# Optimization experiments

Hardware: AMD Instinct MI355X
Metric: run time of the kernel (lower is better)

Reference implementation:

```python
import jax, jax.numpy as jnp
import numpy as np

LEAKAGE = 0.9
RADIUS = 0.1
AVG_DEGREE = 6


def setup_inputs() -> dict:
    key = jax.random.key(0)
    k1, k2, k3, k4, k5 = jax.random.split(key, 5)
    B, T, I, N, O = 16, 2048, 32, 2048, 32
    input_sequence = jax.random.normal(k1, (B, T, I), dtype=jnp.float32)
    # sparse reservoir matrix, uniform(-1,1) with density avg_degree/N, scaled to spectral radius
    A = jax.random.uniform(k2, (N, N), minval=-1.0, maxval=1.0, dtype=jnp.float32)
    mask = jax.random.uniform(k3, (N, N)) < (AVG_DEGREE / N)
    A = jnp.where(mask, A, 0.0)
    # approximate spectral normalization (power-iteration-free surrogate scale)
    A = A * (RADIUS / jnp.max(jnp.abs(jnp.linalg.eigvals(A))).astype(jnp.float32))
    Win = (RADIUS) * (2.0 * jax.random.uniform(k4, (N, I), dtype=jnp.float32) - 1.0)
    Wout_w = jax.random.normal(k5, (O, N), dtype=jnp.float32) / np.sqrt(N)
    return {"input_sequence": input_sequence, "Win": Win, "A": A, "Wout_w": Wout_w, "washout_len": 64}


def reference(input_sequence, Win, A, Wout_w, washout_len):
    # input projection for all timesteps at once (noise_std = 0.0)
    inp = jnp.einsum('bti,ni->btn', input_sequence, Win)  # [B, T, N]
    B = input_sequence.shape[0]
    N = A.shape[0]
    h0 = jnp.zeros((B, N), dtype=input_sequence.dtype)
    At = A.T

    def step(h, u_t):
        # h: [B, N], u_t: [B, N]
        h_new = (1.0 - LEAKAGE) * h + LEAKAGE * jnp.tanh(h @ At + u_t)
        return h_new, h_new

    _, hs = jax.lax.scan(step, h0, jnp.swapaxes(inp, 0, 1))  # hs: [T, B, N]
    hs = jnp.swapaxes(hs, 0, 1)  # [B, T, N]
    h_list = hs[:, washout_len - 1:]  # keep steps i >= washout_len - 1
    return jnp.einsum('btn,on->bto', h_list, Wout_w)
```

## Files before the change

### kernel.cpp

```cpp
#include <hip/hip_runtime.h>
#include <stdint.h>

#define BB 16
#define TT 2048
#define NI 32
#define NN 2048
#define NO 32
#define WASH 64
#define TO (TT - WASH + 1)
#define W 24
#define WT 24
#define CH 16
#define HBST 2048
#define HBROW 4096
#define UROWB 4132
#define U2OFF 65536
#define C1OFF 131712
#define LDS_BYTES (C1OFF + 8192)

typedef short bfvec __attribute__((ext_vector_type(8)));
typedef float f4_t  __attribute__((ext_vector_type(4)));

__device__ inline unsigned short f2bf(float f) {
  unsigned int u = __builtin_bit_cast(unsigned int, f);
  unsigned int r = u + 0x7fffu + ((u >> 16) & 1u);
  return (unsigned short)(r >> 16);
}
__device__ inline float bf2f(unsigned short s) {
  unsigned int u = ((unsigned int)s) << 16;
  return __builtin_bit_cast(float, u);
}
__device__ inline float tanh_fast(float x) {
  x = fminf(15.f, fmaxf(-15.f, x));
  float e = __expf(x + x);
  float r = __builtin_amdgcn_rcpf(e + 1.0f);
  return (e - 1.0f) * r;
}

__global__ void build_ell(const float* __restrict__ A, uint32_t* __restrict__ ell,
                          uint32_t* __restrict__ deg) {
  int gw = (int)((blockIdx.x * blockDim.x + threadIdx.x) >> 6);
  int lane = (int)(threadIdx.x & 63);
  if (gw >= NN) return;
  const float* row = A + (size_t)gw * NN;
  int base = 0;
  for (int c = 0; c < NN; c += 64) {
    float v = row[c + lane];
    bool nz = (v != 0.0f);
    unsigned long long mask = __ballot(nz);
    int pre = __popcll(mask & ((1ull << lane) - 1ull));
    if (nz) {
      int idx = base + pre;
      if (idx < W) {
        uint32_t packed = (((uint32_t)f2bf(v)) << 16) | (uint32_t)((c + lane) * 4);
        ell[(size_t)gw * W + idx] = packed;
      }
    }
    base += __popcll(mask);
  }
  int d = base < W ? base : W;
  if (lane == 0) deg[gw] = (uint32_t)d;
  for (int k = d + lane; k < W; k += 64) ell[(size_t)gw * W + k] = 0u;
}

__global__ void sortperm(const uint32_t* __restrict__ deg, uint32_t* __restrict__ perm,
                         uint32_t* __restrict__ invp) {
  __shared__ int dg[NN];
  int tid = (int)threadIdx.x;
  for (int i = tid; i < NN; i += 256) dg[i] = (int)deg[i];
  __syncthreads();
  int r = (int)blockIdx.x * 256 + tid;
  int d = dg[r];
  int rank = 0;
  for (int j = 0; j < NN; ++j) {
    int dj = dg[j];
    rank += (dj < d) || (dj == d && j < r);
  }
  perm[rank] = (uint32_t)r;
  invp[r] = (uint32_t)rank;
}

__global__ void pairsort(const uint32_t* __restrict__ deg, const uint32_t* __restrict__ perm,
                         uint32_t* __restrict__ pairrank, uint32_t* __restrict__ pp) {
  __shared__ int ps[1024];
  int tid = (int)threadIdx.x;
  for (int i = tid; i < 1024; i += 256) {
    int d0 = (int)deg[perm[i]]; if (d0 > W) d0 = W;
    int d1 = (int)deg[perm[2047 - i]]; if (d1 > W) d1 = W;
    int s = d0 + d1; if (s > WT) s = WT;
    ps[i] = s;
  }
  __syncthreads();
  int p = (int)blockIdx.x * 256 + tid;
  int s = ps[p];
  int rank = 0;
  for (int j = 0; j < 1024; ++j) {
    int sj = ps[j];
    rank += (sj < s) || (sj == s && j < p);
  }
  pairrank[p] = (uint32_t)rank;
  pp[rank] = (uint32_t)p;
}

__device__ inline int rank2pos(int r, const uint32_t* pairrank) {
  return (r < 1024) ? (2 * (int)pairrank[r]) : (2 * (int)pairrank[2047 - r] + 1);
}

__device__ inline int c1pos(int t) {
  int l = t & 31, h = t >> 5;
  return (h << 5) | ((17 * l + 5 * h) & 31);
}

__global__ void build_pairs(const uint32_t* __restrict__ ell, const uint32_t* __restrict__ deg,
                            const uint32_t* __restrict__ perm, const uint32_t* __restrict__ invp,
                            const uint32_t* __restrict__ pairrank, const uint32_t* __restrict__ pp,
                            uint32_t* __restrict__ pa, uint32_t* __restrict__ pva,
                            uint32_t* __restrict__ pvb, uint32_t* __restrict__ wavecnt) {
  int blk = (int)blockIdx.x;
  int lane = (int)threadIdx.x;
  int half = lane >> 5;
  int t = blk * 64 + lane;
  int p = (int)pp[t];
  uint32_t a0_[WT], a1_[WT], u_[WT], w_[WT];
  int cnt = 0;
  {
    int ro = (int)perm[p];
    int d = (int)deg[ro]; if (d > W) d = W;
    for (int k = 0; k < d && cnt < WT; ++k) {
      uint32_t e = ell[(size_t)ro * W + k];
      int pos = rank2pos((int)invp[(e & 0xffffu) >> 2], pairrank);
      a0_[cnt] = (uint32_t)(pos * 2);
      a1_[cnt] = (uint32_t)(c1pos(pos >> 1) * 4 + (pos & 1) * 2);
      u_[cnt] = e & 0xffff0000u;
      w_[cnt] = 0u;
      ++cnt;
    }
    ro = (int)perm[2047 - p];
    d = (int)deg[ro]; if (d > W) d = W;
    for (int k = 0; k < d && cnt < WT; ++k) {
      uint32_t e = ell[(size_t)ro * W + k];
      int pos = rank2pos((int)invp[(e & 0xffffu) >> 2], pairrank);
      a0_[cnt] = (uint32_t)(pos * 2);
      a1_[cnt] = (uint32_t)(c1pos(pos >> 1) * 4 + (pos & 1) * 2);
      u_[cnt] = 0u;
      w_[cnt] = e & 0xffff0000u;
      ++cnt;
    }
  }
  int m = cnt;
  #pragma unroll
  for (int off = 32; off; off >>= 1) m = max(m, __shfl_xor(m, off));
  int S = m < 8 ? 8 : (m > 24 ? 24 : m);
  if (lane == 0) wavecnt[blk] = (uint32_t)S;

  uint32_t sa[WT], su[WT], sw[WT];
  for (int s = 0; s < WT; ++s) {
    sa[s] = ((uint32_t)((lane + s) & 31)) << 2;
    su[s] = 0u; sw[s] = 0u;
  }
  uint32_t used = 0;
  int rem = cnt;
  for (int s = 0; s < S; ++s) {
    int copy = s & 1;
    unsigned long long occ = 0ull;
    bool placed = false;
    const int R = 4;
    for (int r = 0; r < R; ++r) {
      bool last = (r == R - 1);
      bool urgent = (rem >= S - s);
      int pk = -1, pb = 32;
      if (!placed && rem > 0) {
        for (int k = 0; k < WT; ++k) {
          if (k >= cnt) break;
          if ((used >> k) & 1u) continue;
          int b = copy ? (int)((a1_[k] >> 2) & 31u) : (int)((a0_[k] >> 2) & 31u);
          if (!((occ >> (half * 32 + b)) & 1ull)) { pk = k; pb = b; break; }
        }
        if (pk < 0 && last && urgent) {
          for (int k = 0; k < WT; ++k) {
            if (k >= cnt) break;
            if (!((used >> k) & 1u)) {
              pk = k;
              pb = copy ? (int)((a1_[k] >> 2) & 31u) : (int)((a0_[k] >> 2) & 31u);
              break;
            }
          }
        }
      }
      int shift = (s * 19 + r * 7) & 31;
      for (int b = 0; b < 32; ++b) {
        unsigned long long mb = __ballot(pb == b);
        if (!mb) continue;
        for (int h = 0; h < 2; ++h) {
          uint32_t mh = (uint32_t)(mb >> (h * 32));
          if (!mh) continue;
          bool freeb = !((occ >> (h * 32 + b)) & 1ull);
          uint32_t mhr = (mh >> shift) | (mh << ((32 - shift) & 31));
          int winpos = __ffs(mhr) - 1;
          int winlane = ((winpos + shift) & 31) + h * 32;
          if (freeb) occ |= 1ull << (h * 32 + b);
          if (pb == b && half == h && !placed) {
            bool win = (lane == winlane);
            if ((freeb && win) || (last && urgent)) {
              placed = true;
              used |= 1u << (unsigned)pk;
              sa[s] = copy ? a1_[pk] : a0_[pk];
              su[s] = u_[pk]; sw[s] = w_[pk];
              rem--;
            }
          }
        }
      }
    }
    if (!placed) {
      int pick = (lane + s) & 31;
      for (int j = 0; j < 32; ++j) {
        int b = (lane + s + j) & 31;
        if (!((occ >> (half * 32 + b)) & 1ull)) { pick = b; break; }
      }
      sa[s] = ((uint32_t)pick) << 2;
    }
  }
  for (int k = 0; k < WT; ++k) {
    pa[(size_t)t * WT + k] = sa[k];
    pva[(size_t)t * WT + k] = su[k];
    pvb[(size_t)t * WT + k] = sw[k];
  }
}

__global__ void build_frags(const float* __restrict__ Win, const float* __restrict__ Wout,
                            const uint32_t* __restrict__ perm, const uint32_t* __restrict__ pp,
                            uint32_t* __restrict__ winf, uint32_t* __restrict__ woutf) {
  int f = (int)(blockIdx.x * blockDim.x + threadIdx.x);
  if (f < 32768) {
    int reg = f & 3, lane = (f >> 2) & 63, ntg = f >> 8;
    int n = (ntg << 4) + (lane & 15);
    int k = ((lane >> 4) << 3) + reg * 2;
    int p = (int)pp[n >> 1];
    int np = (int)perm[(n & 1) ? (2047 - p) : p];
    uint32_t lo = f2bf(Win[(size_t)np * NI + k]);
    uint32_t hi = f2bf(Win[(size_t)np * NI + k + 1]);
    winf[f] = lo | (hi << 16);
  } else {
    int g = f - 32768;
    int reg = g & 3, lane = (g >> 2) & 63, kt = (g >> 8) & 63, ot = g >> 14;
    int o = (ot << 4) + (lane & 15);
    int n = (kt << 5) + ((lane >> 4) << 3) + reg * 2;
    int p = (int)pp[n >> 1];
    int n0 = (int)perm[p];
    int n1 = (int)perm[2047 - p];
    uint32_t lo = f2bf(Wout[(size_t)o * NN + n0]);
    uint32_t hi = f2bf(Wout[(size_t)o * NN + n1]);
    woutf[g] = lo | (hi << 16);
  }
}

#define ENT(K)                                                                       \
  {                                                                                  \
    float hv = bf2f(*(const unsigned short*)(smem + ((((K) & 1) ? po1 : po0)) + ea##K)); \
    y0 = __builtin_fmaf(__builtin_bit_cast(float, va##K), hv, y0);                   \
    y1 = __builtin_fmaf(__builtin_bit_cast(float, vb##K), hv, y1);                   \
  }

#define ENTS8  ENT(0) ENT(1) ENT(2) ENT(3) ENT(4) ENT(5) ENT(6) ENT(7)
#define ENTS9  ENTS8  ENT(8)
#define ENTS10 ENTS9  ENT(9)
#define ENTS11 ENTS10 ENT(10)
#define ENTS12 ENTS11 ENT(11)
#define ENTS13 ENTS12 ENT(12)
#define ENTS14 ENTS13 ENT(13)
#define ENTS15 ENTS14 ENT(14)
#define ENTS16 ENTS15 ENT(15)
#define ENTS17 ENTS16 ENT(16)
#define ENTS18 ENTS17 ENT(17)
#define ENTS19 ENTS18 ENT(18)
#define ENTS20 ENTS19 ENT(19)
#define ENTS21 ENTS20 ENT(20)
#define ENTS22 ENTS21 ENT(21)
#define ENTS23 ENTS22 ENT(22)
#define ENTS24 ENTS23 ENT(23)

#define STEPLOOP(ENTS)                                                               \
  _Pragma("unroll 1")                                                                \
  for (int tt = 0; tt < CH; ++tt) {                                                  \
    const int po0 = ((tt + CH - 1) & (CH - 1)) << 12;                                \
    const int po1 = C1OFF + (((tt + 1) & 1) << 12);                                  \
    uint32_t uw = *(const uint32_t*)(smem + u2a + tt * UROWB);                       \
    float y0 = bf2f((unsigned short)(uw & 0xffffu));                                 \
    float y1 = bf2f((unsigned short)(uw >> 16));                                     \
    ENTS                                                                             \
    float hn0 = 0.1f * h0 + 0.9f * tanh_fast(y0);                                    \
    float hn1 = 0.1f * h1 + 0.9f * tanh_fast(y1);                                    \
    uint32_t wpk = (uint32_t)f2bf(hn0) | ((uint32_t)f2bf(hn1) << 16);                \
    *(uint32_t*)(smem + hwa + (tt << 12)) = wpk;                                     \
    *(uint32_t*)(smem + c1wa + ((tt & 1) << 12)) = wpk;                              \
    h0 = hn0; h1 = hn1;                                                              \
    __syncthreads();                                                                 \
  }

__global__ __launch_bounds__(1024, 1) void rec_kernel(
    const float* __restrict__ x,
    const uint32_t* __restrict__ pa, const uint32_t* __restrict__ pva,
    const uint32_t* __restrict__ pvb, const uint32_t* __restrict__ wavecnt,
    const uint32_t* __restrict__ winf, const uint32_t* __restrict__ woutf,
    float* __restrict__ out) {
  extern __shared__ char smem[];
  unsigned short* hb = (unsigned short*)smem;
  float* oscratch = (float*)(smem + U2OFF);

  const int tid = (int)threadIdx.x;
  const int b = (int)blockIdx.x;
  const int lane = tid & 63;
  const int wv = tid >> 6;
  const int la15 = lane & 15;
  const int lg = lane >> 4;
  const int u2a = U2OFF + (tid << 2);
  const int hwa = tid << 2;
  const int c1wa = C1OFF + (((tid >> 5 << 5) | ((17 * (tid & 31) + 5 * (tid >> 5)) & 31)) << 2);

  int cnt = __builtin_amdgcn_readfirstlane((int)wavecnt[wv]);

  uint32_t ea0, ea1, ea2, ea3, ea4, ea5, ea6, ea7, ea8, ea9, ea10, ea11,
           ea12, ea13, ea14, ea15, ea16, ea17, ea18, ea19, ea20, ea21, ea22, ea23;
  uint32_t va0, va1, va2, va3, va4, va5, va6, va7, va8, va9, va10, va11,
           va12, va13, va14, va15, va16, va17, va18, va19, va20, va21, va22, va23;
  uint32_t vb0, vb1, vb2, vb3, vb4, vb5, vb6, vb7, vb8, vb9, vb10, vb11,
           vb12, vb13, vb14, vb15, vb16, vb17, vb18, vb19, vb20, vb21, vb22, vb23;
  {
    const uint4* qa = (const uint4*)(pa + (size_t)tid * WT);
    const uint4* qv = (const uint4*)(pva + (size_t)tid * WT);
    const uint4* qw = (const uint4*)(pvb + (size_t)tid * WT);
    uint4 A0 = qa[0], A1 = qa[1], A2 = qa[2], A3 = qa[3], A4 = qa[4], A5 = qa[5];
    uint4 V0 = qv[0], V1 = qv[1], V2 = qv[2], V3 = qv[3], V4 = qv[4], V5 = qv[5];
    uint4 B0 = qw[0], B1 = qw[1], B2 = qw[2], B3 = qw[3], B4 = qw[4], B5 = qw[5];
    ea0 = A0.x; ea1 = A0.y; ea2 = A0.z; ea3 = A0.w;
    ea4 = A1.x; ea5 = A1.y; ea6 = A1.z; ea7 = A1.w;
    ea8 = A2.x; ea9 = A2.y; ea10 = A2.z; ea11 = A2.w;
    ea12 = A3.x; ea13 = A3.y; ea14 = A3.z; ea15 = A3.w;
    ea16 = A4.x; ea17 = A4.y; ea18 = A4.z; ea19 = A4.w;
    ea20 = A5.x; ea21 = A5.y; ea22 = A5.z; ea23 = A5.w;
    va0 = V0.x; va1 = V0.y; va2 = V0.z; va3 = V0.w;
    va4 = V1.x; va5 = V1.y; va6 = V1.z; va7 = V1.w;
    va8 = V2.x; va9 = V2.y; va10 = V2.z; va11 = V2.w;
    va12 = V3.x; va13 = V3.y; va14 = V3.z; va15 = V3.w;
    va16 = V4.x; va17 = V4.y; va18 = V4.z; va19 = V4.w;
    va20 = V5.x; va21 = V5.y; va22 = V5.z; va23 = V5.w;
    vb0 = B0.x; vb1 = B0.y; vb2 = B0.z; vb3 = B0.w;
    vb4 = B1.x; vb5 = B1.y; vb6 = B1.z; vb7 = B1.w;
    vb8 = B2.x; vb9 = B2.y; vb10 = B2.z; vb11 = B2.w;
    vb12 = B3.x; vb13 = B3.y; vb14 = B3.z; vb15 = B3.w;
    vb16 = B4.x; vb17 = B4.y; vb18 = B4.z; vb19 = B4.w;
    vb20 = B5.x; vb21 = B5.y; vb22 = B5.z; vb23 = B5.w;
  }

  *(uint32_t*)(smem + 15 * HBROW + (tid << 2)) = 0u;
  *(uint32_t*)(smem + C1OFF + 4096 + (tid << 2)) = 0u;
  float h0 = 0.0f, h1 = 0.0f;

  for (int c = 0; c < TT / CH; ++c) {
    const int t0 = c * CH;

    {
      const float* xp = x + ((size_t)b * TT + (t0 + la15)) * NI + (lg << 3);
      float4 x0 = *(const float4*)xp;
      float4 x1 = *(const float4*)(xp + 4);
      union { unsigned short u16[8]; bfvec v; } af;
      af.u16[0]=f2bf(x0.x); af.u16[1]=f2bf(x0.y); af.u16[2]=f2bf(x0.z); af.u16[3]=f2bf(x0.w);
      af.u16[4]=f2bf(x1.x); af.u16[5]=f2bf(x1.y); af.u16[6]=f2bf(x1.z); af.u16[7]=f2bf(x1.w);
      #pragma unroll
      for (int nt = 0; nt < 8; ++nt) {
        int ntg = (wv << 3) + nt;
        union { uint4 q; bfvec v; } bw;
        bw.q = *(const uint4*)(winf + (((size_t)ntg * 64 + lane) << 2));
        f4_t acc = {0.f, 0.f, 0.f, 0.f};
        acc = __builtin_amdgcn_mfma_f32_16x16x32_bf16(bw.v, af.v, acc, 0, 0, 0);
        int dw = (ntg << 3) + (lg << 1);
        uint32_t w0 = (uint32_t)f2bf(acc[0]) | ((uint32_t)f2bf(acc[1]) << 16);
        uint32_t w1 = (uint32_t)f2bf(acc[2]) | ((uint32_t)f2bf(acc[3]) << 16);
        char* ub = smem + U2OFF + la15 * UROWB + (dw << 2);
        *(uint32_t*)(ub) = w0;
        *(uint32_t*)(ub + 4) = w1;
      }
    }
    __syncthreads();

    asm volatile("" : "+s"(cnt));
    if      (cnt <= 8)  { STEPLOOP(ENTS8)  }
    else if (cnt == 9)  { STEPLOOP(ENTS9)  }
    else if (cnt == 10) { STEPLOOP(ENTS10) }
    else if (cnt == 11) { STEPLOOP(ENTS11) }
    else if (cnt == 12) { STEPLOOP(ENTS12) }
    else if (cnt == 13) { STEPLOOP(ENTS13) }
    else if (cnt == 14) { STEPLOOP(ENTS14) }
    else if (cnt == 15) { STEPLOOP(ENTS15) }
    else if (cnt == 16) { STEPLOOP(ENTS16) }
    else if (cnt == 17) { STEPLOOP(ENTS17) }
    else if (cnt == 18) { STEPLOOP(ENTS18) }
    else if (cnt == 19) { STEPLOOP(ENTS19) }
    else if (cnt == 20) { STEPLOOP(ENTS20) }
    else if (cnt == 21) { STEPLOOP(ENTS21) }
    else if (cnt == 22) { STEPLOOP(ENTS22) }
    else if (cnt == 23) { STEPLOOP(ENTS23) }
    else                { STEPLOOP(ENTS24) }

    {
      f4_t oa0 = {0.f,0.f,0.f,0.f}, oa1 = {0.f,0.f,0.f,0.f};
      #pragma unroll
      for (int k4 = 0; k4 < 4; ++k4) {
        int kt = (wv << 2) + k4;
        union { uint4 q; bfvec v; } ha, w0, w1;
        ha.q = *(const uint4*)(hb + (size_t)la15 * HBST + (kt << 5) + (lg << 3));
        w0.q = *(const uint4*)(woutf + (((size_t)(kt) * 64 + lane) << 2));
        w1.q = *(const uint4*)(woutf + (((size_t)(64 + kt) * 64 + lane) << 2));
        oa0 = __builtin_amdgcn_mfma_f32_16x16x32_bf16(ha.v, w0.v, oa0, 0, 0, 0);
        oa1 = __builtin_amdgcn_mfma_f32_16x16x32_bf16(ha.v, w1.v, oa1, 0, 0, 0);
      }
      float* os = oscratch + (wv << 9);
      int tb = lg << 2;
      #pragma unroll
      for (int r = 0; r < 4; ++r) os[(tb + r) * 32 + la15] = oa0[r];
      #pragma unroll
      for (int r = 0; r < 4; ++r) os[(tb + r) * 32 + 16 + la15] = oa1[r];
    }
    __syncthreads();
    if (tid < 512) {
      float s = 0.0f;
      #pragma unroll
      for (int w2 = 0; w2 < 16; ++w2) s += oscratch[(w2 << 9) + tid];
      int tg = t0 + (tid >> 5);
      if (tg >= WASH - 1)
        out[((size_t)b * TO + (tg - (WASH - 1))) * NO + (tid & 31)] = s;
    }
    __syncthreads();
  }
}

extern "C" void kernel_launch(void* const* d_in, const int* in_sizes, int n_in,
                              void* d_out, int out_size, void* d_ws, size_t ws_size,
                              hipStream_t stream) {
  (void)in_sizes; (void)n_in; (void)out_size; (void)ws_size;
  const float* x    = (const float*)d_in[0];
  const float* Win  = (const float*)d_in[1];
  const float* A    = (const float*)d_in[2];
  const float* Wout = (const float*)d_in[3];
  float* out = (float*)d_out;

  char* ws = (char*)d_ws;
  uint32_t* ell      = (uint32_t*)(ws);
  uint32_t* deg      = (uint32_t*)(ws + 196608);
  uint32_t* perm     = (uint32_t*)(ws + 204800);
  uint32_t* invp     = (uint32_t*)(ws + 212992);
  uint32_t* pairrank = (uint32_t*)(ws + 221184);
  uint32_t* pp       = (uint32_t*)(ws + 225280);
  uint32_t* wavecnt  = (uint32_t*)(ws + 229376);
  uint32_t* pa       = (uint32_t*)(ws + 229504);
  uint32_t* pva      = (uint32_t*)(ws + 327808);
  uint32_t* pvb      = (uint32_t*)(ws + 426112);
  uint32_t* winf     = (uint32_t*)(ws + 524416);
  uint32_t* woutf    = (uint32_t*)(ws + 655488);

  hipFuncSetAttribute((const void*)rec_kernel,
                      hipFuncAttributeMaxDynamicSharedMemorySize, 160 * 1024);

  hipLaunchKernelGGL(build_ell, dim3(512), dim3(256), 0, stream, A, ell, deg);
  hipLaunchKernelGGL(sortperm, dim3(8), dim3(256), 0, stream, deg, perm, invp);
  hipLaunchKernelGGL(pairsort, dim3(4), dim3(256), 0, stream, deg, perm, pairrank, pp);
  hipLaunchKernelGGL(build_pairs, dim3(16), dim3(64), 0, stream,
                     ell, deg, perm, invp, pairrank, pp, pa, pva, pvb, wavecnt);
  hipLaunchKernelGGL(build_frags, dim3(256), dim3(256), 0, stream, Win, Wout, perm, pp, winf, woutf);
  hipLaunchKernelGGL(rec_kernel, dim3(16), dim3(1024), LDS_BYTES, stream,
                     x, pa, pva, pvb, wavecnt, winf, woutf, out);
}
```

Baseline: 2.931 ms.

## Use a single double-buffered state row and a separate padded history buffer

The per-chunk state history used to double as the gather source. Each step also wrote a second, bank-swizzled copy of the state that odd entries read from. Now the gather reads from one ping-pong double-buffered state row, and each step writes a second copy into a padded history buffer used for the output MFMA projection. The swizzled copy and the pair builder's split of entries between the two copies are removed, which simplifies addressing. The output scratch rows are also padded to reduce bank conflicts. The risk is more LDS bank conflicts in the gather, since every entry now hits the same unswizzled buffer.

```diff
diff --git a/kernel.cpp b/kernel.cpp
--- a/kernel.cpp
+++ b/kernel.cpp
@@ -11,12 +11,13 @@
 #define W 24
 #define WT 24
 #define CH 16
-#define HBST 2048
-#define HBROW 4096
+#define U2OFF 8192
 #define UROWB 4132
-#define U2OFF 65536
-#define C1OFF 131712
-#define LDS_BYTES (C1OFF + 8192)
+#define HBT_OFF 74368
+#define HBTROW 4148
+#define OSW 35
+#define OSWAVE 560
+#define LDS_BYTES (HBT_OFF + CH*HBTROW)
 
 typedef short bfvec __attribute__((ext_vector_type(8)));
 typedef float f4_t  __attribute__((ext_vector_type(4)));
@@ -106,11 +107,6 @@
   return (r < 1024) ? (2 * (int)pairrank[r]) : (2 * (int)pairrank[2047 - r] + 1);
 }
 
-__device__ inline int c1pos(int t) {
-  int l = t & 31, h = t >> 5;
-  return (h << 5) | ((17 * l + 5 * h) & 31);
-}
-
 __global__ void build_pairs(const uint32_t* __restrict__ ell, const uint32_t* __restrict__ deg,
                             const uint32_t* __restrict__ perm, const uint32_t* __restrict__ invp,
                             const uint32_t* __restrict__ pairrank, const uint32_t* __restrict__ pp,
@@ -121,7 +117,7 @@
   int half = lane >> 5;
   int t = blk * 64 + lane;
   int p = (int)pp[t];
-  uint32_t a0_[WT], a1_[WT], u_[WT], w_[WT];
+  uint32_t a_[WT], u_[WT], w_[WT];
   int cnt = 0;
   {
     int ro = (int)perm[p];
@@ -129,8 +125,7 @@
     for (int k = 0; k < d && cnt < WT; ++k) {
       uint32_t e = ell[(size_t)ro * W + k];
       int pos = rank2pos((int)invp[(e & 0xffffu) >> 2], pairrank);
-      a0_[cnt] = (uint32_t)(pos * 2);
-      a1_[cnt] = (uint32_t)(c1pos(pos >> 1) * 4 + (pos & 1) * 2);
+      a_[cnt] = (uint32_t)(pos * 2);
       u_[cnt] = e & 0xffff0000u;
       w_[cnt] = 0u;
       ++cnt;
@@ -140,8 +135,7 @@
     for (int k = 0; k < d && cnt < WT; ++k) {
       uint32_t e = ell[(size_t)ro * W + k];
       int pos = rank2pos((int)invp[(e & 0xffffu) >> 2], pairrank);
-      a0_[cnt] = (uint32_t)(pos * 2);
-      a1_[cnt] = (uint32_t)(c1pos(pos >> 1) * 4 + (pos & 1) * 2);
+      a_[cnt] = (uint32_t)(pos * 2);
       u_[cnt] = 0u;
       w_[cnt] = e & 0xffff0000u;
       ++cnt;
@@ -161,7 +155,6 @@
   uint32_t used = 0;
   int rem = cnt;
   for (int s = 0; s < S; ++s) {
-    int copy = s & 1;
     unsigned long long occ = 0ull;
     bool placed = false;
     const int R = 4;
@@ -173,7 +166,7 @@
         for (int k = 0; k < WT; ++k) {
           if (k >= cnt) break;
           if ((used >> k) & 1u) continue;
-          int b = copy ? (int)((a1_[k] >> 2) & 31u) : (int)((a0_[k] >> 2) & 31u);
+          int b = (int)((a_[k] >> 2) & 31u);
           if (!((occ >> (half * 32 + b)) & 1ull)) { pk = k; pb = b; break; }
         }
         if (pk < 0 && last && urgent) {
@@ -181,7 +174,7 @@
             if (k >= cnt) break;
             if (!((used >> k) & 1u)) {
               pk = k;
-              pb = copy ? (int)((a1_[k] >> 2) & 31u) : (int)((a0_[k] >> 2) & 31u);
+              pb = (int)((a_[k] >> 2) & 31u);
               break;
             }
           }
@@ -204,7 +197,7 @@
             if ((freeb && win) || (last && urgent)) {
               placed = true;
               used |= 1u << (unsigned)pk;
-              sa[s] = copy ? a1_[pk] : a0_[pk];
+              sa[s] = a_[pk];
               su[s] = u_[pk]; sw[s] = w_[pk];
               rem--;
             }
@@ -257,7 +250,7 @@
 
 #define ENT(K)                                                                       \
   {                                                                                  \
-    float hv = bf2f(*(const unsigned short*)(smem + ((((K) & 1) ? po1 : po0)) + ea##K)); \
+    float hv = bf2f(*(const unsigned short*)(smem + po0 + ea##K));                   \
     y0 = __builtin_fmaf(__builtin_bit_cast(float, va##K), hv, y0);                   \
     y1 = __builtin_fmaf(__builtin_bit_cast(float, vb##K), hv, y1);                   \
   }
@@ -283,8 +276,7 @@
 #define STEPLOOP(ENTS)                                                               \
   _Pragma("unroll 1")                                                                \
   for (int tt = 0; tt < CH; ++tt) {                                                  \
-    const int po0 = ((tt + CH - 1) & (CH - 1)) << 12;                                \
-    const int po1 = C1OFF + (((tt + 1) & 1) << 12);                                  \
+    const int po0 = ((tt + 1) & 1) << 12;                                            \
     uint32_t uw = *(const uint32_t*)(smem + u2a + tt * UROWB);                       \
     float y0 = bf2f((unsigned short)(uw & 0xffffu));                                 \
     float y1 = bf2f((unsigned short)(uw >> 16));                                     \
@@ -292,8 +284,8 @@
     float hn0 = 0.1f * h0 + 0.9f * tanh_fast(y0);                                    \
     float hn1 = 0.1f * h1 + 0.9f * tanh_fast(y1);                                    \
     uint32_t wpk = (uint32_t)f2bf(hn0) | ((uint32_t)f2bf(hn1) << 16);                \
-    *(uint32_t*)(smem + hwa + (tt << 12)) = wpk;                                     \
-    *(uint32_t*)(smem + c1wa + ((tt & 1) << 12)) = wpk;                              \
+    *(uint32_t*)(smem + hwa + ((tt & 1) << 12)) = wpk;                               \
+    *(uint32_t*)(smem + hbtwa + tt * HBTROW) = wpk;                                  \
     h0 = hn0; h1 = hn1;                                                              \
     __syncthreads();                                                                 \
   }
@@ -305,7 +297,6 @@
     const uint32_t* __restrict__ winf, const uint32_t* __restrict__ woutf,
     float* __restrict__ out) {
   extern __shared__ char smem[];
-  unsigned short* hb = (unsigned short*)smem;
   float* oscratch = (float*)(smem + U2OFF);
 
   const int tid = (int)threadIdx.x;
@@ -316,7 +307,7 @@
   const int lg = lane >> 4;
   const int u2a = U2OFF + (tid << 2);
   const int hwa = tid << 2;
-  const int c1wa = C1OFF + (((tid >> 5 << 5) | ((17 * (tid & 31) + 5 * (tid >> 5)) & 31)) << 2);
+  const int hbtwa = HBT_OFF + (tid << 2);
 
   int cnt = __builtin_amdgcn_readfirstlane((int)wavecnt[wv]);
 
@@ -353,8 +344,7 @@
     vb20 = B5.x; vb21 = B5.y; vb22 = B5.z; vb23 = B5.w;
   }
 
-  *(uint32_t*)(smem + 15 * HBROW + (tid << 2)) = 0u;
-  *(uint32_t*)(smem + C1OFF + 4096 + (tid << 2)) = 0u;
+  *(uint32_t*)(smem + 4096 + (tid << 2)) = 0u;
   float h0 = 0.0f, h1 = 0.0f;
 
   for (int c = 0; c < TT / CH; ++c) {
@@ -409,24 +399,25 @@
       for (int k4 = 0; k4 < 4; ++k4) {
         int kt = (wv << 2) + k4;
         union { uint4 q; bfvec v; } ha, w0, w1;
-        ha.q = *(const uint4*)(hb + (size_t)la15 * HBST + (kt << 5) + (lg << 3));
+        ha.q = *(const uint4*)(smem + HBT_OFF + la15 * HBTROW + (kt << 6) + (lg << 4));
         w0.q = *(const uint4*)(woutf + (((size_t)(kt) * 64 + lane) << 2));
         w1.q = *(const uint4*)(woutf + (((size_t)(64 + kt) * 64 + lane) << 2));
         oa0 = __builtin_amdgcn_mfma_f32_16x16x32_bf16(ha.v, w0.v, oa0, 0, 0, 0);
         oa1 = __builtin_amdgcn_mfma_f32_16x16x32_bf16(ha.v, w1.v, oa1, 0, 0, 0);
       }
-      float* os = oscratch + (wv << 9);
+      float* os = oscratch + wv * OSWAVE;
       int tb = lg << 2;
       #pragma unroll
-      for (int r = 0; r < 4; ++r) os[(tb + r) * 32 + la15] = oa0[r];
+      for (int r = 0; r < 4; ++r) os[(tb + r) * OSW + la15] = oa0[r];
       #pragma unroll
-      for (int r = 0; r < 4; ++r) os[(tb + r) * 32 + 16 + la15] = oa1[r];
+      for (int r = 0; r < 4; ++r) os[(tb + r) * OSW + 16 + la15] = oa1[r];
     }
     __syncthreads();
     if (tid < 512) {
       float s = 0.0f;
+      int ro = (tid >> 5) * OSW + (tid & 31);
       #pragma unroll
-      for (int w2 = 0; w2 < 16; ++w2) s += oscratch[(w2 << 9) + tid];
+      for (int w2 = 0; w2 < 16; ++w2) s += oscratch[w2 * OSWAVE + ro];
       int tg = t0 + (tid >> 5);
       if (tg >= WASH - 1)
         out[((size_t)b * TO + (tg - (WASH - 1))) * NO + (tid & 31)] = s;
```

Result: no change. 2.915 ms (-0.5%).
